# Optimization experiments

Measured on AMD Instinct MI355X. Metric: run time of the kernel, lower is better.

Reference implementation:

```python
import jax, jax.numpy as jnp
import numpy as np

EPS = 1e-6

def _log_g(x):
    # log of continuous g(x) = where(x>=0, x+0.5, sigmoid(x)) from minGRU paper
    return jnp.where(x >= 0, jnp.log(jax.nn.relu(x) + 0.5), -jax.nn.softplus(-x))

def setup_inputs() -> dict:
    key = jax.random.key(0)
    ks = jax.random.split(key, 4)
    B, S, D, E = 4, 2048, 1024, 8
    scale = D ** -0.5
    return {
        "inputs": jax.random.normal(ks[0], (B, S, D), dtype=jnp.float32),
        "norm_weight": jnp.ones((D,), jnp.float32),
        "router_w": jax.random.normal(ks[1], (E, D), jnp.float32) * scale,
        "router_b": jnp.zeros((E,), jnp.float32),
        "w_hg": jax.random.normal(ks[2], (E, 2 * D, D), jnp.float32) * scale,
        "w_out": jax.random.normal(ks[3], (E, D, D), jnp.float32) * scale,
    }

def reference(inputs, norm_weight, router_w, router_b, w_hg, w_out):
    D = inputs.shape[-1]
    # --- RMSNorm ---
    x = inputs * jax.lax.rsqrt(jnp.mean(inputs * inputs, axis=-1, keepdims=True) + EPS) * norm_weight
    # --- SMEAR: per-sample soft merge of expert weights via mean-pooled routing ---
    probs = jax.nn.softmax(jnp.mean(x, axis=1) @ router_w.T + router_b, axis=-1)  # [B,E]
    W_hg = jnp.einsum('be,ekd->bkd', probs, w_hg)    # [B,2D,D] merged to_hidden_and_gate
    W_out = jnp.einsum('be,eod->bod', probs, w_out)  # [B,D,D]  merged to_out
    # --- minGRU with merged weights (log-space parallel scan, no initial state) ---
    hg = jnp.einsum('bsd,bkd->bsk', x, W_hg)         # [B,S,2D]
    hidden, gate = hg[..., :D], hg[..., D:]
    log_coeffs = -jax.nn.softplus(gate)                      # log(1 - z_t)
    log_values = -jax.nn.softplus(-gate) + _log_g(hidden)    # log z_t + log g(h~_t)
    a_star = jnp.cumsum(log_coeffs, axis=1)
    log_h = a_star + jax.lax.cumlogsumexp(log_values - a_star, axis=1)
    h = jnp.exp(log_h)                               # [B,S,D] recurrent states
    new_state = h[:, -1:]                            # [B,1,D]
    out = jnp.einsum('bsk,bok->bso', h, W_out)       # proj_out
    aux_loss = jnp.zeros((), inputs.dtype)
    return (out + inputs, new_state, aux_loss)
```

## Files before the change

kernel.cpp:

```cpp
#include <hip/hip_runtime.h>
#include <hip/hip_bf16.h>
#include <hip/hip_fp16.h>

#define B_  4
#define S_  2048
#define D_  1024
#define E_  8
#define K2_ 2048

#define CHUNKS 64
#define CLEN   32

typedef __attribute__((ext_vector_type(8))) short short8;
typedef __attribute__((ext_vector_type(4))) float floatx4;

__device__ __forceinline__ void gld16(const void* g, const void* l) {
    __builtin_amdgcn_global_load_lds(
        (const __attribute__((address_space(1))) unsigned int*)g,
        (__attribute__((address_space(3))) unsigned int*)l, 16, 0, 0);
}

__device__ __forceinline__ unsigned short f2bf(float f) {
    unsigned int u = __float_as_uint(f);
    u += 0x7fffu + ((u >> 16) & 1u);
    return (unsigned short)(u >> 16);
}

__global__ void rmsnorm_k(const float* __restrict__ in, const float* __restrict__ nw,
                          __hip_bfloat16* __restrict__ x) {
    int b = blockIdx.y, s = blockIdx.x, t = threadIdx.x;
    const float4* row = (const float4*)(in + ((size_t)b * S_ + s) * D_);
    float4 v = row[t];
    float ss = v.x * v.x + v.y * v.y + v.z * v.z + v.w * v.w;
#pragma unroll
    for (int o = 32; o > 0; o >>= 1) ss += __shfl_down(ss, o, 64);
    __shared__ float ls[4];
    if ((t & 63) == 0) ls[t >> 6] = ss;
    __syncthreads();
    float tot = ls[0] + ls[1] + ls[2] + ls[3];
    float rs = rsqrtf(tot * (1.0f / (float)D_) + 1e-6f);
    float4 w = ((const float4*)nw)[t];
    ushort4 o;
    o.x = f2bf(v.x * rs * w.x); o.y = f2bf(v.y * rs * w.y);
    o.z = f2bf(v.z * rs * w.z); o.w = f2bf(v.w * rs * w.w);
    ((ushort4*)(x + ((size_t)b * S_ + s) * D_))[t] = o;
}

__global__ void xsum_k(const __hip_bfloat16* __restrict__ x, float* __restrict__ xs) {
    int d = blockIdx.x * 256 + threadIdx.x;
    int b = blockIdx.y;
    int s0 = blockIdx.z * 128;
    const __hip_bfloat16* p = x + ((size_t)b * S_ + s0) * D_ + d;
    float acc = 0.0f;
#pragma unroll 4
    for (int s = 0; s < 128; s++) { acc += __bfloat162float(*p); p += D_; }
    atomicAdd(&xs[b * D_ + d], acc);
}

__global__ void router_k(const float* __restrict__ xs, const float* __restrict__ rw,
                         const float* __restrict__ rb, float* __restrict__ probs,
                         float* __restrict__ aux) {
    int t = threadIdx.x;
    if (t == 255) *aux = 0.0f;
    int pair = t >> 3, sub = t & 7;
    int b = pair >> 3, e = pair & 7;
    float acc = 0.0f;
#pragma unroll 8
    for (int d = sub; d < D_; d += 8) acc += xs[b * D_ + d] * rw[e * D_ + d];
#pragma unroll
    for (int o = 4; o > 0; o >>= 1) acc += __shfl_down(acc, o, 8);
    __shared__ float lg[32];
    if (sub == 0) lg[pair] = acc * (1.0f / (float)S_) + rb[e];
    __syncthreads();
    if (t < 4) {
        float m = -1e30f;
        for (int e2 = 0; e2 < 8; e2++) m = fmaxf(m, lg[t * 8 + e2]);
        float ssum = 0.0f; float ex[8];
        for (int e2 = 0; e2 < 8; e2++) { ex[e2] = expf(lg[t * 8 + e2] - m); ssum += ex[e2]; }
        for (int e2 = 0; e2 < 8; e2++) probs[t * 8 + e2] = ex[e2] / ssum;
    }
}

__global__ void mix_k(const float* __restrict__ probs, const float* __restrict__ whg_e,
                      const float* __restrict__ wout_e, __hip_bfloat16* __restrict__ Whg,
                      __hip_bfloat16* __restrict__ Wout) {
    __shared__ float P[32];
    int t = threadIdx.x;
    if (t < 32) P[t] = probs[t];
    __syncthreads();
    size_t i4 = (size_t)blockIdx.x * 256 + t;
    const size_t T1q = (size_t)K2_ * D_ / 4;
    const size_t T2q = (size_t)D_ * D_ / 4;
    float4 a0 = {0,0,0,0}, a1 = {0,0,0,0}, a2 = {0,0,0,0}, a3 = {0,0,0,0};
    if (i4 < T1q) {
        const float4* src = (const float4*)whg_e;
#pragma unroll
        for (int e = 0; e < 8; e++) {
            float4 wv = src[(size_t)e * T1q + i4];
            float p0 = P[e], p1 = P[8 + e], p2 = P[16 + e], p3 = P[24 + e];
            a0.x += p0 * wv.x; a0.y += p0 * wv.y; a0.z += p0 * wv.z; a0.w += p0 * wv.w;
            a1.x += p1 * wv.x; a1.y += p1 * wv.y; a1.z += p1 * wv.z; a1.w += p1 * wv.w;
            a2.x += p2 * wv.x; a2.y += p2 * wv.y; a2.z += p2 * wv.z; a2.w += p2 * wv.w;
            a3.x += p3 * wv.x; a3.y += p3 * wv.y; a3.z += p3 * wv.z; a3.w += p3 * wv.w;
        }
        ushort4* dst = (ushort4*)Whg;
        ushort4 o;
        o.x = f2bf(a0.x); o.y = f2bf(a0.y); o.z = f2bf(a0.z); o.w = f2bf(a0.w);
        dst[0 * T1q + i4] = o;
        o.x = f2bf(a1.x); o.y = f2bf(a1.y); o.z = f2bf(a1.z); o.w = f2bf(a1.w);
        dst[1 * T1q + i4] = o;
        o.x = f2bf(a2.x); o.y = f2bf(a2.y); o.z = f2bf(a2.z); o.w = f2bf(a2.w);
        dst[2 * T1q + i4] = o;
        o.x = f2bf(a3.x); o.y = f2bf(a3.y); o.z = f2bf(a3.z); o.w = f2bf(a3.w);
        dst[3 * T1q + i4] = o;
    } else {
        size_t j4 = i4 - T1q;
        const float4* src = (const float4*)wout_e;
#pragma unroll
        for (int e = 0; e < 8; e++) {
            float4 wv = src[(size_t)e * T2q + j4];
            float p0 = P[e], p1 = P[8 + e], p2 = P[16 + e], p3 = P[24 + e];
            a0.x += p0 * wv.x; a0.y += p0 * wv.y; a0.z += p0 * wv.z; a0.w += p0 * wv.w;
            a1.x += p1 * wv.x; a1.y += p1 * wv.y; a1.z += p1 * wv.z; a1.w += p1 * wv.w;
            a2.x += p2 * wv.x; a2.y += p2 * wv.y; a2.z += p2 * wv.z; a2.w += p2 * wv.w;
            a3.x += p3 * wv.x; a3.y += p3 * wv.y; a3.z += p3 * wv.z; a3.w += p3 * wv.w;
        }
        ushort4* dst = (ushort4*)Wout;
        ushort4 o;
        o.x = f2bf(a0.x); o.y = f2bf(a0.y); o.z = f2bf(a0.z); o.w = f2bf(a0.w);
        dst[0 * T2q + j4] = o;
        o.x = f2bf(a1.x); o.y = f2bf(a1.y); o.z = f2bf(a1.z); o.w = f2bf(a1.w);
        dst[1 * T2q + j4] = o;
        o.x = f2bf(a2.x); o.y = f2bf(a2.y); o.z = f2bf(a2.z); o.w = f2bf(a2.w);
        dst[2 * T2q + j4] = o;
        o.x = f2bf(a3.x); o.y = f2bf(a3.y); o.z = f2bf(a3.z); o.w = f2bf(a3.w);
        dst[3 * T2q + j4] = o;
    }
}

__global__ __launch_bounds__(512, 2) void gemm_hg_cv(
    const __hip_bfloat16* __restrict__ A, const __hip_bfloat16* __restrict__ Bm,
    __half2* __restrict__ cv) {
    const int K = D_;
    int bz = blockIdx.z;
    A  += (size_t)bz * S_ * D_;
    Bm += (size_t)bz * K2_ * D_;
    __half2* CV = cv + (size_t)bz * S_ * D_;
    int id = blockIdx.x;
    int sw = (id & 7) * 8 + (id >> 3);
    int m0 = (sw >> 3) * 256, n0 = (sw & 7) * 128;
    __shared__ __hip_bfloat16 lA[2][256][64];
    __shared__ __hip_bfloat16 lBh[2][128][64];
    __shared__ __hip_bfloat16 lBg[2][128][64];
    int t = threadIdx.x;
    int w = t >> 6, lane = t & 63;
    int lm = lane & 15, quad = lane >> 4;
    int wr = w >> 1, wc = w & 1;
    floatx4 acch[4][4] = {};
    floatx4 accg[4][4] = {};
    int srow = lane >> 3;
    int swzb = ((lane & 7) ^ srow) * 16;

    const __hip_bfloat16* Bh = Bm;
    const __hip_bfloat16* Bg = Bm + (size_t)D_ * K;

    const char* pA[4]; const char* pBhp[2]; const char* pBgp[2];
#pragma unroll
    for (int it = 0; it < 4; it++)
        pA[it] = (const char*)(A + (size_t)(m0 + (w * 4 + it) * 8 + srow) * K) + swzb;
#pragma unroll
    for (int it = 0; it < 2; it++) {
        pBhp[it] = (const char*)(Bh + (size_t)(n0 + (w * 2 + it) * 8 + srow) * K) + swzb;
        pBgp[it] = (const char*)(Bg + (size_t)(n0 + (w * 2 + it) * 8 + srow) * K) + swzb;
    }

    auto stage = [&](int bb) {
#pragma unroll
        for (int it = 0; it < 4; it++) {
            gld16(pA[it], &lA[bb][(w * 4 + it) * 8][0]);
            pA[it] += 128;
        }
#pragma unroll
        for (int it = 0; it < 2; it++) {
            gld16(pBhp[it], &lBh[bb][(w * 2 + it) * 8][0]); pBhp[it] += 128;
            gld16(pBgp[it], &lBg[bb][(w * 2 + it) * 8][0]); pBgp[it] += 128;
        }
    };

    stage(0);
    int cur = 0;
    for (int k0 = 0; k0 < K; k0 += 64) {
        if (k0 + 64 < K) {
            stage(cur ^ 1);
            asm volatile("s_waitcnt vmcnt(8)" ::: "memory");
        } else {
            asm volatile("s_waitcnt vmcnt(0)" ::: "memory");
        }
        __builtin_amdgcn_s_barrier();
#pragma unroll
        for (int kk = 0; kk < 64; kk += 32) {
            short8 af[4], bh[4], bg[4];
            int p = (((kk >> 3) + quad) ^ (lm & 7)) * 8;
#pragma unroll
            for (int i = 0; i < 4; i++)
                af[i] = *(const short8*)(&lA[cur][wr * 64 + i * 16 + lm][p]);
#pragma unroll
            for (int j = 0; j < 4; j++) {
                bh[j] = *(const short8*)(&lBh[cur][wc * 64 + j * 16 + lm][p]);
                bg[j] = *(const short8*)(&lBg[cur][wc * 64 + j * 16 + lm][p]);
            }
            __builtin_amdgcn_s_setprio(1);
#pragma unroll
            for (int i = 0; i < 4; i++)
#pragma unroll
                for (int j = 0; j < 4; j++) {
                    acch[i][j] = __builtin_amdgcn_mfma_f32_16x16x32_bf16(
                        af[i], bh[j], acch[i][j], 0, 0, 0);
                    accg[i][j] = __builtin_amdgcn_mfma_f32_16x16x32_bf16(
                        af[i], bg[j], accg[i][j], 0, 0, 0);
                }
            __builtin_amdgcn_s_setprio(0);
        }
        asm volatile("s_waitcnt lgkmcnt(0)" ::: "memory");
        __builtin_amdgcn_s_barrier();
        cur ^= 1;
    }
#pragma unroll
    for (int i = 0; i < 4; i++) {
#pragma unroll
        for (int j = 0; j < 4; j++) {
#pragma unroll
            for (int r = 0; r < 4; r++) {
                int m = m0 + wr * 64 + i * 16 + quad * 4 + r;
                int n = n0 + wc * 64 + j * 16 + lm;
                float hid = acch[i][j][r];
                float g   = accg[i][j][r];
                float eg  = expf(g);
                float c   = 1.0f / (1.0f + eg);
                float sg  = 1.0f - c;
                float gfn = (hid >= 0.0f) ? (hid + 0.5f)
                                          : (1.0f / (1.0f + expf(-hid)));
                CV[(size_t)m * D_ + n] = __floats2half2_rn(c, sg * gfn);
            }
        }
    }
}

#define TM 128
#define TN 128
#define TBK 64
__global__ __launch_bounds__(256) void gemm_bf16_bt(
    const __hip_bfloat16* __restrict__ A, const __hip_bfloat16* __restrict__ Bm,
    float* __restrict__ C, const float* __restrict__ R,
    int M, int N, int K, size_t sa, size_t sb, size_t sc, size_t sr) {
    int bz = blockIdx.z;
    A += (size_t)bz * sa; Bm += (size_t)bz * sb; C += (size_t)bz * sc;
    if (R) R += (size_t)bz * sr;
    int id = blockIdx.x;
    int sw = (id & 7) * 16 + (id >> 3);
    int m0 = (sw >> 3) * TM, n0 = (sw & 7) * TN;
    __shared__ __hip_bfloat16 lA[2][TM][TBK];
    __shared__ __hip_bfloat16 lB[2][TN][TBK];
    int t = threadIdx.x;
    int w = t >> 6, lane = t & 63;
    int lm = lane & 15, quad = lane >> 4;
    int wr = w >> 1, wc = w & 1;
    floatx4 acc[4][4] = {};
    int srow = lane >> 3;
    int swzb = ((lane & 7) ^ srow) * 16;

    const char* pA[4]; const char* pB[4];
#pragma unroll
    for (int it = 0; it < 4; it++) {
        pA[it] = (const char*)(A + (size_t)(m0 + (w * 4 + it) * 8 + srow) * K) + swzb;
        pB[it] = (const char*)(Bm + (size_t)(n0 + (w * 4 + it) * 8 + srow) * K) + swzb;
    }

    auto stage = [&](int bb) {
#pragma unroll
        for (int it = 0; it < 4; it++) {
            gld16(pA[it], &lA[bb][(w * 4 + it) * 8][0]); pA[it] += 128;
            gld16(pB[it], &lB[bb][(w * 4 + it) * 8][0]); pB[it] += 128;
        }
    };

    stage(0);
    int cur = 0;
    for (int k0 = 0; k0 < K; k0 += TBK) {
        if (k0 + TBK < K) {
            stage(cur ^ 1);
            asm volatile("s_waitcnt vmcnt(8)" ::: "memory");
        } else {
            asm volatile("s_waitcnt vmcnt(0)" ::: "memory");
        }
        __builtin_amdgcn_s_barrier();
#pragma unroll
        for (int kk = 0; kk < TBK; kk += 32) {
            short8 af[4], bf[4];
            int p = (((kk >> 3) + quad) ^ (lm & 7)) * 8;
#pragma unroll
            for (int i = 0; i < 4; i++)
                af[i] = *(const short8*)(&lA[cur][wr * 64 + i * 16 + lm][p]);
#pragma unroll
            for (int j = 0; j < 4; j++)
                bf[j] = *(const short8*)(&lB[cur][wc * 64 + j * 16 + lm][p]);
            __builtin_amdgcn_s_setprio(1);
#pragma unroll
            for (int i = 0; i < 4; i++)
#pragma unroll
                for (int j = 0; j < 4; j++)
                    acc[i][j] = __builtin_amdgcn_mfma_f32_16x16x32_bf16(
                        af[i], bf[j], acc[i][j], 0, 0, 0);
            __builtin_amdgcn_s_setprio(0);
        }
        asm volatile("s_waitcnt lgkmcnt(0)" ::: "memory");
        __builtin_amdgcn_s_barrier();
        cur ^= 1;
    }
#pragma unroll
    for (int i = 0; i < 4; i++) {
#pragma unroll
        for (int j = 0; j < 4; j++) {
#pragma unroll
            for (int r = 0; r < 4; r++) {
                int m = m0 + wr * 64 + i * 16 + quad * 4 + r;
                int n = n0 + wc * 64 + j * 16 + lm;
                float v = acc[i][j][r];
                if (R) v += R[(size_t)m * N + n];
                C[(size_t)m * N + n] = v;
            }
        }
    }
}

__global__ void scanA_k(const __half2* __restrict__ cv, float* __restrict__ Cc,
                        float* __restrict__ Vc) {
    int c = blockIdx.x, b = blockIdx.y, t = threadIdx.x;
    const float4* p = (const float4*)(cv + (size_t)(b * S_ + c * CLEN) * D_) + t;
    float P0 = 1, P1 = 1, P2 = 1, P3 = 1;
    float V0 = 0, V1 = 0, V2 = 0, V3 = 0;
#pragma unroll 4
    for (int s = 0; s < CLEN; s++) {
        float4 raw = p[(size_t)s * (D_ / 4)];
        const __half2* e = (const __half2*)&raw;
        float c0 = __low2float(e[0]), v0 = __high2float(e[0]);
        float c1 = __low2float(e[1]), v1 = __high2float(e[1]);
        float c2 = __low2float(e[2]), v2 = __high2float(e[2]);
        float c3 = __low2float(e[3]), v3 = __high2float(e[3]);
        P0 *= c0; V0 = fmaf(c0, V0, v0);
        P1 *= c1; V1 = fmaf(c1, V1, v1);
        P2 *= c2; V2 = fmaf(c2, V2, v2);
        P3 *= c3; V3 = fmaf(c3, V3, v3);
    }
    size_t q = ((size_t)(b * CHUNKS + c)) * (D_ / 4) + t;
    ((float4*)Cc)[q] = make_float4(P0, P1, P2, P3);
    ((float4*)Vc)[q] = make_float4(V0, V1, V2, V3);
}

__global__ void scanC_k(const __half2* __restrict__ cv, const float* __restrict__ Cc,
                        const float* __restrict__ Vc,
                        __hip_bfloat16* __restrict__ hout, float* __restrict__ ns) {
    int c = blockIdx.x, b = blockIdx.y, t = threadIdx.x;
    float h0 = 0, h1 = 0, h2 = 0, h3 = 0;
#pragma unroll 4
    for (int cc = 0; cc < c; cc++) {
        size_t q = ((size_t)(b * CHUNKS + cc)) * (D_ / 4) + t;
        float4 C4 = ((const float4*)Cc)[q];
        float4 V4 = ((const float4*)Vc)[q];
        h0 = fmaf(C4.x, h0, V4.x); h1 = fmaf(C4.y, h1, V4.y);
        h2 = fmaf(C4.z, h2, V4.z); h3 = fmaf(C4.w, h3, V4.w);
    }
    const float4* p = (const float4*)(cv + (size_t)(b * S_ + c * CLEN) * D_) + t;
    ushort4* hq = (ushort4*)(hout + (size_t)(b * S_ + c * CLEN) * D_) + t;
#pragma unroll 4
    for (int s = 0; s < CLEN; s++) {
        float4 raw = p[(size_t)s * (D_ / 4)];
        const __half2* e = (const __half2*)&raw;
        h0 = fmaf(__low2float(e[0]), h0, __high2float(e[0]));
        h1 = fmaf(__low2float(e[1]), h1, __high2float(e[1]));
        h2 = fmaf(__low2float(e[2]), h2, __high2float(e[2]));
        h3 = fmaf(__low2float(e[3]), h3, __high2float(e[3]));
        ushort4 o;
        o.x = f2bf(h0); o.y = f2bf(h1); o.z = f2bf(h2); o.w = f2bf(h3);
        hq[(size_t)s * (D_ / 4)] = o;
    }
    if (c == CHUNKS - 1)
        ((float4*)(ns + (size_t)b * D_))[t] = make_float4(h0, h1, h2, h3);
}

extern "C" void kernel_launch(void* const* d_in, const int* in_sizes, int n_in,
                              void* d_out_v, int out_size, void* d_ws, size_t ws_size,
                              hipStream_t stream) {
    const float* inputs = (const float*)d_in[0];
    const float* nw     = (const float*)d_in[1];
    const float* rw     = (const float*)d_in[2];
    const float* rb     = (const float*)d_in[3];
    const float* whg_e  = (const float*)d_in[4];
    const float* wout_e = (const float*)d_in[5];
    float* out = (float*)d_out_v;

    float* ws = (float*)d_ws;
    __half2*        cv      = (__half2*)ws;
    __hip_bfloat16* x_bf    = (__hip_bfloat16*)(ws + 8388608);
    __hip_bfloat16* h_bf    = (__hip_bfloat16*)(ws + 12582912);
    __hip_bfloat16* Whg_bf  = (__hip_bfloat16*)(ws + 16777216);
    __hip_bfloat16* Wout_bf = (__hip_bfloat16*)(ws + 20971520);
    float* xsum  = ws + 23068672;
    float* probs = ws + 23072768;
    float* Cc    = ws + 23072800;
    float* Vc    = ws + 23334944;

    hipMemsetAsync(xsum, 0, (size_t)B_ * D_ * sizeof(float), stream);

    rmsnorm_k<<<dim3(S_, B_), 256, 0, stream>>>(inputs, nw, x_bf);
    xsum_k<<<dim3(D_ / 256, B_, 16), 256, 0, stream>>>(x_bf, xsum);
    router_k<<<1, 256, 0, stream>>>(xsum, rw, rb, probs,
                                    out + (size_t)B_ * S_ * D_ + (size_t)B_ * D_);
    mix_k<<<3072, 256, 0, stream>>>(probs, whg_e, wout_e, Whg_bf, Wout_bf);

    gemm_hg_cv<<<dim3(64, 1, B_), 512, 0, stream>>>(x_bf, Whg_bf, cv);

    scanA_k<<<dim3(CHUNKS, B_), 256, 0, stream>>>(cv, Cc, Vc);
    scanC_k<<<dim3(CHUNKS, B_), 256, 0, stream>>>(
        cv, Cc, Vc, h_bf, out + (size_t)B_ * S_ * D_);

    gemm_bf16_bt<<<dim3(128, 1, B_), 256, 0, stream>>>(
        h_bf, Wout_bf, out, inputs, S_, D_, D_,
        (size_t)S_ * D_, (size_t)D_ * D_, (size_t)S_ * D_, (size_t)S_ * D_);
}
```

Baseline: 304.4 us.

## Interleave global-to-LDS prefetch with MFMA phases in hidden/gate GEMM

Splits each 64-wide K tile of the hidden/gate GEMM into four phases and issues half of the next tile's global-to-LDS loads inside each of the first two phases. Each phase is bracketed by barriers and sched_barriers, so loads are spread across the compute instead of being issued in one burst. It also makes the output GEMM's final stores nontemporal to reduce cache pollution. The extra barriers per tile and the vmcnt(0) wait at the top of each iteration may cost more than the overlap gains. The loop hardcodes 16 iterations, so it assumes K=1024.

```diff
diff --git a/kernel.cpp b/kernel.cpp
--- a/kernel.cpp
+++ b/kernel.cpp
@@ -174,55 +174,58 @@
         pBgp[it] = (const char*)(Bg + (size_t)(n0 + (w * 2 + it) * 8 + srow) * K) + swzb;
     }
 
-    auto stage = [&](int bb) {
-#pragma unroll
-        for (int it = 0; it < 4; it++) {
-            gld16(pA[it], &lA[bb][(w * 4 + it) * 8][0]);
-            pA[it] += 128;
-        }
-#pragma unroll
-        for (int it = 0; it < 2; it++) {
-            gld16(pBhp[it], &lBh[bb][(w * 2 + it) * 8][0]); pBhp[it] += 128;
-            gld16(pBgp[it], &lBg[bb][(w * 2 + it) * 8][0]); pBgp[it] += 128;
+    auto stage_part = [&](int bb, int part) {
+        if (part == 0) {
+            gld16(pA[0], &lA[bb][(w * 4 + 0) * 8][0]); pA[0] += 128;
+            gld16(pA[1], &lA[bb][(w * 4 + 1) * 8][0]); pA[1] += 128;
+            gld16(pBhp[0], &lBh[bb][(w * 2 + 0) * 8][0]); pBhp[0] += 128;
+            gld16(pBgp[0], &lBg[bb][(w * 2 + 0) * 8][0]); pBgp[0] += 128;
+        } else {
+            gld16(pA[2], &lA[bb][(w * 4 + 2) * 8][0]); pA[2] += 128;
+            gld16(pA[3], &lA[bb][(w * 4 + 3) * 8][0]); pA[3] += 128;
+            gld16(pBhp[1], &lBh[bb][(w * 2 + 1) * 8][0]); pBhp[1] += 128;
+            gld16(pBgp[1], &lBg[bb][(w * 2 + 1) * 8][0]); pBgp[1] += 128;
         }
     };
 
-    stage(0);
+    stage_part(0, 0); stage_part(0, 1);
     int cur = 0;
-    for (int k0 = 0; k0 < K; k0 += 64) {
-        if (k0 + 64 < K) {
-            stage(cur ^ 1);
-            asm volatile("s_waitcnt vmcnt(8)" ::: "memory");
-        } else {
-            asm volatile("s_waitcnt vmcnt(0)" ::: "memory");
-        }
+    for (int kt = 0; kt < 16; kt++) {
+        asm volatile("s_waitcnt vmcnt(0)" ::: "memory");
         __builtin_amdgcn_s_barrier();
-#pragma unroll
-        for (int kk = 0; kk < 64; kk += 32) {
-            short8 af[4], bh[4], bg[4];
-            int p = (((kk >> 3) + quad) ^ (lm & 7)) * 8;
+        bool pre = (kt < 15);
+#pragma unroll
+        for (int p = 0; p < 4; p++) {
+            const int kh = p & 1, bjh = p >> 1;
+            const int off = ((kh * 4 + quad) ^ (lm & 7)) * 16;
+            short8 af[4], bhf[2], bgf[2];
 #pragma unroll
             for (int i = 0; i < 4; i++)
-                af[i] = *(const short8*)(&lA[cur][wr * 64 + i * 16 + lm][p]);
-#pragma unroll
-            for (int j = 0; j < 4; j++) {
-                bh[j] = *(const short8*)(&lBh[cur][wc * 64 + j * 16 + lm][p]);
-                bg[j] = *(const short8*)(&lBg[cur][wc * 64 + j * 16 + lm][p]);
+                af[i] = *(const short8*)((const char*)&lA[cur][wr * 64 + i * 16 + lm][0] + off);
+#pragma unroll
+            for (int jj = 0; jj < 2; jj++) {
+                int j = bjh * 2 + jj;
+                bhf[jj] = *(const short8*)((const char*)&lBh[cur][wc * 64 + j * 16 + lm][0] + off);
+                bgf[jj] = *(const short8*)((const char*)&lBg[cur][wc * 64 + j * 16 + lm][0] + off);
             }
+            if (pre && p < 2) stage_part(cur ^ 1, p);
+            __builtin_amdgcn_s_barrier();
+            asm volatile("s_waitcnt lgkmcnt(0)" ::: "memory");
+            __builtin_amdgcn_sched_barrier(0);
             __builtin_amdgcn_s_setprio(1);
 #pragma unroll
             for (int i = 0; i < 4; i++)
 #pragma unroll
-                for (int j = 0; j < 4; j++) {
+                for (int jj = 0; jj < 2; jj++) {
+                    int j = bjh * 2 + jj;
                     acch[i][j] = __builtin_amdgcn_mfma_f32_16x16x32_bf16(
-                        af[i], bh[j], acch[i][j], 0, 0, 0);
+                        af[i], bhf[jj], acch[i][j], 0, 0, 0);
                     accg[i][j] = __builtin_amdgcn_mfma_f32_16x16x32_bf16(
-                        af[i], bg[j], accg[i][j], 0, 0, 0);
+                        af[i], bgf[jj], accg[i][j], 0, 0, 0);
                 }
             __builtin_amdgcn_s_setprio(0);
-        }
-        asm volatile("s_waitcnt lgkmcnt(0)" ::: "memory");
-        __builtin_amdgcn_s_barrier();
+            __builtin_amdgcn_s_barrier();
+        }
         cur ^= 1;
     }
 #pragma unroll
@@ -327,7 +330,7 @@
                 int n = n0 + wc * 64 + j * 16 + lm;
                 float v = acc[i][j][r];
                 if (R) v += R[(size_t)m * N + n];
-                C[(size_t)m * N + n] = v;
+                __builtin_nontemporal_store(v, &C[(size_t)m * N + n]);
             }
         }
     }
```

Measured after the change: 302.1 us. No clear change (-0.8%).
